# Optimization experiments

Hardware: AMD Instinct MI355X
Metric: run time of the kernel (lower is better)

## Reference

```python
import jax, jax.numpy as jnp
import numpy as np
from jax import lax

LEAK = 0.2
GN_EPS = 1e-5
K_NEIGH = 16
GROUPS = 4


def knn_idx(coor_k, coor_q, k):
    # coor_k: [B,Nk,3], coor_q: [B,Nq,3] -> [B,Nq,k] indices of k nearest in coor_k
    d = (jnp.sum(coor_q * coor_q, -1, keepdims=True)
         - 2.0 * jnp.einsum('bqc,bkc->bqk', coor_q, coor_k)
         + jnp.sum(coor_k * coor_k, -1)[:, None, :])
    _, idx = lax.top_k(-d, k)
    return idx


def graph_feature(coor_q, x_q, coor_k, x_k, k):
    # coor_*: [B,3,N*]; x_q: [B,C,Nq]; x_k: [B,C,Nk] -> [B,2C,Nq,k]
    idx = knn_idx(lax.stop_gradient(coor_k).transpose(0, 2, 1),
                  lax.stop_gradient(coor_q).transpose(0, 2, 1), k)
    B = x_k.shape[0]
    x_k_t = x_k.transpose(0, 2, 1)                      # [B,Nk,C]
    b_idx = jnp.arange(B)[:, None, None]
    nb = x_k_t[b_idx, idx]                              # [B,Nq,k,C]
    nb = nb.transpose(0, 3, 1, 2)                       # [B,C,Nq,k]
    xq = x_q[:, :, :, None]                             # [B,C,Nq,1]
    return jnp.concatenate([nb - xq, jnp.broadcast_to(xq, nb.shape)], axis=1)


def conv_gn_lrelu_max(f, w, gamma, beta):
    # f: [B,Cin,N,k]; w: [Cout,Cin] -> [B,Cout,N] (max over k)
    y = jnp.einsum('oc,bcnk->bonk', w, f)
    B, C, N, Kk = y.shape
    g = y.reshape(B, GROUPS, C // GROUPS, N, Kk)
    mu = g.mean((2, 3, 4), keepdims=True)
    var = g.var((2, 3, 4), keepdims=True)
    g = (g - mu) * lax.rsqrt(var + GN_EPS)
    y = g.reshape(B, C, N, Kk) * gamma[None, :, None, None] + beta[None, :, None, None]
    y = jnp.where(y >= 0, y, LEAK * y)
    return y.max(axis=-1)


def fps(xyz, n):
    # xyz: [B,N,3] -> [B,n] int32 (furthest point sampling, start at index 0)
    B, N, _ = xyz.shape
    d0 = jnp.sum((xyz - xyz[:, :1]) ** 2, -1)           # dist to point 0
    def body(dist, _):
        idx = jnp.argmax(dist, -1)                       # [B]
        nxt = jnp.take_along_axis(xyz, idx[:, None, None], 1)
        dist = jnp.minimum(dist, jnp.sum((xyz - nxt) ** 2, -1))
        return dist, idx
    _, idxs = lax.scan(body, d0, None, length=n - 1)     # [n-1,B]
    first = jnp.zeros((1, B), idxs.dtype)
    return jnp.concatenate([first, idxs], 0).T           # [B,n]


def fps_downsample(coor, x, n):
    # coor: [B,3,N], x: [B,C,N] -> ([B,3,n], [B,C,n])
    idx = fps(lax.stop_gradient(coor).transpose(0, 2, 1), n)
    comb = jnp.concatenate([coor, x], axis=1)            # [B,3+C,N]
    b_idx = jnp.arange(coor.shape[0])[:, None]
    new = comb.transpose(0, 2, 1)[b_idx, idx].transpose(0, 2, 1)
    return new[:, :3], new[:, 3:]


def setup_inputs() -> dict:
    key = jax.random.key(0)
    ks = jax.random.split(key, 16)
    s = 0.1
    return {
        'x': jax.random.normal(ks[0], (32, 2048, 3), jnp.float32),
        'w_in': jax.random.normal(ks[1], (8, 3), jnp.float32) * s,
        'b_in': jnp.zeros((8,), jnp.float32),
        'w1': jax.random.normal(ks[2], (32, 16), jnp.float32) * s,
        'g1': jnp.ones((32,), jnp.float32), 'be1': jnp.zeros((32,), jnp.float32),
        'w2': jax.random.normal(ks[3], (64, 64), jnp.float32) * s,
        'g2': jnp.ones((64,), jnp.float32), 'be2': jnp.zeros((64,), jnp.float32),
        'w3': jax.random.normal(ks[4], (64, 128), jnp.float32) * s,
        'g3': jnp.ones((64,), jnp.float32), 'be3': jnp.zeros((64,), jnp.float32),
        'w4': jax.random.normal(ks[5], (256, 128), jnp.float32) * s,
        'g4': jnp.ones((256,), jnp.float32), 'be4': jnp.zeros((256,), jnp.float32),
        'num0': 512,
        'num1': 128,
    }


def reference(x, w_in, b_in, w1, g1, be1, w2, g2, be2, w3, g3, be3, w4, g4, be4, num0, num1):
    coor = x.transpose(0, 2, 1)                          # [B,3,N]
    f = jnp.einsum('oc,bcn->bon', w_in, coor) + b_in[None, :, None]  # input_trans
    f = graph_feature(coor, f, coor, f, K_NEIGH)         # [B,16,N,k]
    f = conv_gn_lrelu_max(f, w1, g1, be1)                # [B,32,N]
    coor_q, f_q = fps_downsample(coor, f, num0)
    f = graph_feature(coor_q, f_q, coor, f, K_NEIGH)     # [B,64,num0,k]
    f = conv_gn_lrelu_max(f, w2, g2, be2)                # [B,64,num0]
    coor = coor_q
    f = graph_feature(coor, f, coor, f, K_NEIGH)         # [B,128,num0,k]
    f = conv_gn_lrelu_max(f, w3, g3, be3)                # [B,64,num0]
    coor_q, f_q = fps_downsample(coor, f, num1)
    f = graph_feature(coor_q, f_q, coor, f, K_NEIGH)     # [B,128,num1,k]
    f = conv_gn_lrelu_max(f, w4, g4, be4)                # [B,256,num1]
    coor = coor_q
    return coor.transpose(0, 2, 1), f.transpose(0, 2, 1)  # [B,num1,3], [B,num1,256]
```

## Files before the change

### kernel.cpp

```cpp
#include <hip/hip_runtime.h>

#define BB 32
#define NPTS0 2048
#define KNB 16
#define KC 256

constexpr int ilog2c(int n){ int l=0; while(n>1){ n>>=1; ++l; } return l; }

static __device__ __forceinline__ float sq3(float a, float b, float c){
  return __fadd_rn(__fadd_rn(__fmul_rn(a,a),__fmul_rn(b,b)),__fmul_rn(c,c));
}

template<int CTRL, int RM>
static __device__ __forceinline__ float dpp_maxf(float v){
  int s = __builtin_amdgcn_update_dpp(__float_as_int(v), __float_as_int(v), CTRL, RM, 0xF, false);
  return fmaxf(v, __int_as_float(s));
}
template<int CTRL, int RM>
static __device__ __forceinline__ unsigned dpp_minu(unsigned v){
  unsigned s = (unsigned)__builtin_amdgcn_update_dpp((int)v, (int)v, CTRL, RM, 0xF, false);
  return s < v ? s : v;
}

static __device__ __forceinline__ void proj_body(const float* __restrict__ x,
    const float* __restrict__ w, const float* __restrict__ bias, float* __restrict__ f0,
    int blk)
{
  int gid = blk*256 + threadIdx.x;
  if (gid >= BB*NPTS0) return;
  float x0 = x[gid*3+0], x1 = x[gid*3+1], x2 = x[gid*3+2];
  #pragma unroll
  for (int o = 0; o < 8; ++o){
    float acc = __fmul_rn(w[o*3+0], x0);
    acc = __fmaf_rn(w[o*3+1], x1, acc);
    acc = __fmaf_rn(w[o*3+2], x2, acc);
    f0[gid*8+o] = __fadd_rn(acc, bias[o]);
  }
}

#define KDECL(I) float th##I = __builtin_inff(); int ti##I = 0;
#define KINS(I,J) if (th##I < th##J){ float tv=th##I; th##I=th##J; th##J=tv; \
                                      int tj=ti##I; ti##I=ti##J; ti##J=tj; }
#define KST(I) pd[base+I] = th##I; pi[base+I] = (unsigned char)ti##I;

static __device__ __forceinline__ void knn_part_body(const float* __restrict__ qpts,
    const float* __restrict__ kpts, int Nq, int Nk, int nkc,
    float* __restrict__ pd, unsigned char* __restrict__ pi,
    int b, int qcb, int kc, float4* kk4)
{
  int tid = threadIdx.x;
  {
    int j = kc*KC + tid;
    float a = kpts[(b*Nk+j)*3+0];
    float c = kpts[(b*Nk+j)*3+1];
    float d = kpts[(b*Nk+j)*3+2];
    kk4[tid] = make_float4(a, c, d, sq3(a,c,d));
  }
  __syncthreads();
  int q = qcb*256 + tid;
  if (q >= Nq) return;
  float qx = qpts[(b*Nq+q)*3+0], qy = qpts[(b*Nq+q)*3+1], qz = qpts[(b*Nq+q)*3+2];
  float qq = sq3(qx,qy,qz);
  KDECL(0) KDECL(1) KDECL(2) KDECL(3) KDECL(4) KDECL(5) KDECL(6) KDECL(7)
  KDECL(8) KDECL(9) KDECL(10) KDECL(11) KDECL(12) KDECL(13) KDECL(14) KDECL(15)
  for (int j=0;j<KC;j++){
    float4 k4 = kk4[j];
    float dot = __fmul_rn(qx,k4.x);
    dot = __fmaf_rn(qy,k4.y,dot);
    dot = __fmaf_rn(qz,k4.z,dot);
    float d = __fadd_rn(__fsub_rn(qq, __fmul_rn(2.0f,dot)), k4.w);
    if (d < th15){
      th15 = d; ti15 = j;
      KINS(15,14) KINS(14,13) KINS(13,12) KINS(12,11) KINS(11,10) KINS(10,9)
      KINS(9,8) KINS(8,7) KINS(7,6) KINS(6,5) KINS(5,4) KINS(4,3) KINS(3,2)
      KINS(2,1) KINS(1,0)
    }
  }
  size_t base = ((size_t)(b*Nq+q)*nkc + kc)*KNB;
  KST(0) KST(1) KST(2) KST(3) KST(4) KST(5) KST(6) KST(7)
  KST(8) KST(9) KST(10) KST(11) KST(12) KST(13) KST(14) KST(15)
}

#define FPS_LOAD(T) float px##T, py##T, pz##T, d##T; { int i_=T*256+tid; \
  px##T=P[i_*3+0]; py##T=P[i_*3+1]; pz##T=P[i_*3+2]; \
  float dx_=__fsub_rn(px##T,c0x), dy_=__fsub_rn(py##T,c0y), dz_=__fsub_rn(pz##T,c0z); \
  d##T=sq3(dx_,dy_,dz_); bm=fmaxf(bm,d##T); }
#define FPS_MATCH(T) if (d##T == m_w) ci = (unsigned)(T*256 + tid);
#define FPS_OWN(T) if ((idx_w>>8) == T##u){ cx=px##T; cy=py##T; cz=pz##T; }
#define FPS_UPD(T) { float dx_=__fsub_rn(px##T,sx), dy_=__fsub_rn(py##T,sy), dz_=__fsub_rn(pz##T,sz); \
  float nd_=sq3(dx_,dy_,dz_); d##T=fminf(d##T,nd_); nbm=fmaxf(nbm,d##T); }

#define FPS_REDUCE_AND_PICK \
    float v = bm; \
    v = dpp_maxf<0x111, 0xF>(v); \
    v = dpp_maxf<0x112, 0xF>(v); \
    v = dpp_maxf<0x114, 0xF>(v); \
    v = dpp_maxf<0x118, 0xF>(v); \
    v = dpp_maxf<0x142, 0xA>(v); \
    v = dpp_maxf<0x143, 0xC>(v); \
    float m_w = __int_as_float(__builtin_amdgcn_readlane(__float_as_int(v), 63)); \
    unsigned ci = 0xFFFFFFFFu;

#define FPS_MIN_AND_MERGE \
    ci = dpp_minu<0x111, 0xF>(ci); \
    ci = dpp_minu<0x112, 0xF>(ci); \
    ci = dpp_minu<0x114, 0xF>(ci); \
    ci = dpp_minu<0x118, 0xF>(ci); \
    ci = dpp_minu<0x142, 0xA>(ci); \
    ci = dpp_minu<0x143, 0xC>(ci); \
    unsigned idx_w = (unsigned)__builtin_amdgcn_readlane((int)ci, 63); \
    int par = s & 1;

#define FPS_CROSSWAVE \
    __syncthreads(); \
    float4 q0 = *(const float4*)&swp[par][0][0]; float z0 = swp[par][0][4]; \
    float4 q1 = *(const float4*)&swp[par][1][0]; float z1 = swp[par][1][4]; \
    float4 q2 = *(const float4*)&swp[par][2][0]; float z2 = swp[par][2][4]; \
    float4 q3 = *(const float4*)&swp[par][3][0]; float z3 = swp[par][3][4]; \
    float mm = q0.x; unsigned mi = __float_as_uint(q0.y); \
    float sx = q0.z, sy = q0.w, sz = z0; \
    if (q1.x > mm || (q1.x == mm && __float_as_uint(q1.y) < mi)){ \
      mm = q1.x; mi = __float_as_uint(q1.y); sx = q1.z; sy = q1.w; sz = z1; } \
    if (q2.x > mm || (q2.x == mm && __float_as_uint(q2.y) < mi)){ \
      mm = q2.x; mi = __float_as_uint(q2.y); sx = q2.z; sy = q2.w; sz = z2; } \
    if (q3.x > mm || (q3.x == mm && __float_as_uint(q3.y) < mi)){ \
      mm = q3.x; mi = __float_as_uint(q3.y); sx = q3.z; sy = q3.w; sz = z3; } \
    if (tid == 0) oidx[b*S+s] = (int)mi;

static __device__ __forceinline__ void fps8_body(const float* __restrict__ pts,
    int S, int* __restrict__ oidx, int b, float* swpraw)
{
  float (*swp)[4][8] = reinterpret_cast<float(*)[4][8]>(swpraw);
  int tid = threadIdx.x, wid = tid >> 6;
  const float* P = pts + (size_t)b*2048*3;
  float c0x = P[0], c0y = P[1], c0z = P[2];
  float bm = -1.0f;
  FPS_LOAD(0) FPS_LOAD(1) FPS_LOAD(2) FPS_LOAD(3)
  FPS_LOAD(4) FPS_LOAD(5) FPS_LOAD(6) FPS_LOAD(7)
  if (tid == 0) oidx[b*S+0] = 0;
  for (int s=1; s<S; ++s){
    FPS_REDUCE_AND_PICK
    FPS_MATCH(7) FPS_MATCH(6) FPS_MATCH(5) FPS_MATCH(4)
    FPS_MATCH(3) FPS_MATCH(2) FPS_MATCH(1) FPS_MATCH(0)
    FPS_MIN_AND_MERGE
    if (tid == (int)(idx_w & 255u)){
      float cx = px0, cy = py0, cz = pz0;
      FPS_OWN(1) FPS_OWN(2) FPS_OWN(3) FPS_OWN(4) FPS_OWN(5) FPS_OWN(6) FPS_OWN(7)
      float4* wp = (float4*)&swp[par][wid][0];
      *wp = make_float4(m_w, __uint_as_float(idx_w), cx, cy);
      swp[par][wid][4] = cz;
    }
    FPS_CROSSWAVE
    float nbm = -1.0f;
    FPS_UPD(0) FPS_UPD(1) FPS_UPD(2) FPS_UPD(3)
    FPS_UPD(4) FPS_UPD(5) FPS_UPD(6) FPS_UPD(7)
    bm = nbm;
  }
}

static __device__ __forceinline__ void fps2_body(const float* __restrict__ pts,
    int S, int* __restrict__ oidx, int b, float* swpraw)
{
  float (*swp)[4][8] = reinterpret_cast<float(*)[4][8]>(swpraw);
  int tid = threadIdx.x, wid = tid >> 6;
  const float* P = pts + (size_t)b*512*3;
  float c0x = P[0], c0y = P[1], c0z = P[2];
  float bm = -1.0f;
  FPS_LOAD(0) FPS_LOAD(1)
  if (tid == 0) oidx[b*S+0] = 0;
  for (int s=1; s<S; ++s){
    FPS_REDUCE_AND_PICK
    FPS_MATCH(1) FPS_MATCH(0)
    FPS_MIN_AND_MERGE
    if (tid == (int)(idx_w & 255u)){
      float cx = px0, cy = py0, cz = pz0;
      FPS_OWN(1)
      float4* wp = (float4*)&swp[par][wid][0];
      *wp = make_float4(m_w, __uint_as_float(idx_w), cx, cy);
      swp[par][wid][4] = cz;
    }
    FPS_CROSSWAVE
    float nbm = -1.0f;
    FPS_UPD(0) FPS_UPD(1)
    bm = nbm;
  }
}

__global__ __launch_bounds__(256) void fused1_kernel(const float* __restrict__ x,
    const float* __restrict__ w_in, const float* __restrict__ b_in,
    float* __restrict__ f0, float* __restrict__ pd1, unsigned char* __restrict__ pi1,
    int* __restrict__ fidx0)
{
  __shared__ __align__(16) char sm[4096];
  int bid = blockIdx.x;
  if (bid < 32){
    fps8_body(x, 512, fidx0, bid, (float*)sm);
  } else if (bid < 32+2048){
    int r = bid - 32;
    int b = r & 31; int rest = r >> 5;
    knn_part_body(x, x, 2048, 2048, 8, pd1, pi1, b, rest & 7, rest >> 3, (float4*)sm);
  } else {
    proj_body(x, w_in, b_in, f0, bid - 2080);
  }
}

__global__ __launch_bounds__(256) void fused2_kernel(const float* __restrict__ coorq1,
    const float* __restrict__ x,
    float* __restrict__ pd2, unsigned char* __restrict__ pi2,
    float* __restrict__ pd3, unsigned char* __restrict__ pi3,
    int* __restrict__ fidx1)
{
  __shared__ __align__(16) char sm[4096];
  int bid = blockIdx.x;
  if (bid < 32){
    fps2_body(coorq1, 128, fidx1, bid, (float*)sm);
  } else if (bid < 32+512){
    int r = bid - 32;
    int b = r & 31; int rest = r >> 5;
    knn_part_body(coorq1, x, 512, 2048, 8, pd2, pi2, b, rest & 1, rest >> 1, (float4*)sm);
  } else {
    int r = bid - 544;
    int b = r & 31; int rest = r >> 5;
    knn_part_body(coorq1, coorq1, 512, 512, 2, pd3, pi3, b, rest & 1, rest >> 1, (float4*)sm);
  }
}

__global__ __launch_bounds__(256) void knn_part_kernel(const float* __restrict__ qpts,
    const float* __restrict__ kpts, int Nq, int Nk,
    float* __restrict__ pd, unsigned char* __restrict__ pi)
{
  __shared__ __align__(16) float4 kk4[KC];
  knn_part_body(qpts, kpts, Nq, Nk, gridDim.z, pd, pi,
                blockIdx.x, blockIdx.y, blockIdx.z, kk4);
}

__global__ __launch_bounds__(256) void knn_merge_kernel(const float* __restrict__ pd,
    const unsigned char* __restrict__ pi, int Nq, int nkc, int* __restrict__ oidx)
{
  int gid = blockIdx.x*256 + threadIdx.x;
  if (gid >= BB*Nq) return;
  float th[KNB]; int ti[KNB];
  #pragma unroll
  for (int i=0;i<KNB;i++){ th[i] = __builtin_inff(); ti[i] = 0; }
  size_t base = (size_t)gid*nkc*KNB;
  for (int kc=0;kc<nkc;kc++){
    size_t cb = base + (size_t)kc*KNB;
    for (int i=0;i<KNB;i++){
      float d = pd[cb+i];
      if (d >= th[KNB-1]) break;
      int j = kc*KC + (int)pi[cb+i];
      th[KNB-1] = d; ti[KNB-1] = j;
      #pragma unroll
      for (int m=KNB-1;m>0;--m){
        if (th[m] < th[m-1]){
          float tv=th[m]; th[m]=th[m-1]; th[m-1]=tv;
          int tj=ti[m]; ti[m]=ti[m-1]; ti[m-1]=tj;
        }
      }
    }
  }
  #pragma unroll
  for (int i=0;i<KNB;i++) oidx[gid*KNB + i] = ti[i];
}

template<int C, int O, bool DIFF>
__global__ __launch_bounds__(256) void gemv_kernel(const float* __restrict__ fin,
    const float* __restrict__ W, float* __restrict__ out, int Npts)
{
  constexpr int NT = O/8;
  constexpr int LNT = ilog2c(NT);
  int gid = blockIdx.x*256 + threadIdx.x;
  if (gid >= BB*Npts*NT) return;
  int tile = gid & (NT-1);
  int pn = gid >> LNT;
  const float* frow = fin + pn*C;
  float f[C];
  #pragma unroll
  for (int c=0;c<C;c++) f[c] = frow[c];
  float acc[8];
  const float* wbase = W + (tile*8)*(2*C);
  #pragma unroll
  for (int oo=0;oo<8;oo++){
    const float* wrow = wbase + oo*(2*C);
    float a = 0.f;
    #pragma unroll
    for (int c=0;c<C;c++){
      float wv = DIFF ? __fsub_rn(wrow[C+c], wrow[c]) : wrow[c];
      a = __fmaf_rn(wv, f[c], a);
    }
    acc[oo] = a;
  }
  float* orow = out + pn*O + tile*8;
  #pragma unroll
  for (int oo=0;oo<8;oo++) orow[oo] = acc[oo];
}

template<int O>
__global__ __launch_bounds__(256) void stats_kernel(const float* __restrict__ A,
    const float* __restrict__ Bq, const int* __restrict__ idx, int Nq, int Nk,
    double* __restrict__ part)
{
  constexpr int O4 = O/4;
  constexpr int LO4 = ilog2c(O4);
  int b = blockIdx.x, g = blockIdx.y, split = blockIdx.z;
  int nsplit = gridDim.z;
  int qlen = Nq / nsplit;
  int q0 = split * qlen;
  int tid = threadIdx.x;
  int total = qlen * KNB * O4;
  double s1 = 0.0, s2 = 0.0;
  for (int s = tid; s < total; s += 256){
    int oin = s & (O4-1);
    int rest = s >> LO4;
    int kk = rest & (KNB-1);
    int q = q0 + (rest >> 4);
    int j = idx[(b*Nq+q)*KNB + kk];
    float y = A[(b*Nk+j)*O + g*O4 + oin] + Bq[(b*Nq+q)*O + g*O4 + oin];
    s1 += (double)y;
    s2 += (double)y * (double)y;
  }
  #pragma unroll
  for (int m=32;m>0;m>>=1){ s1 += __shfl_down(s1,m); s2 += __shfl_down(s2,m); }
  __shared__ double sh1[4], sh2[4];
  int lane = tid & 63, w = tid >> 6;
  if (lane == 0){ sh1[w]=s1; sh2[w]=s2; }
  __syncthreads();
  if (tid == 0){
    double t1 = (sh1[0]+sh1[1])+(sh1[2]+sh1[3]);
    double t2 = (sh2[0]+sh2[1])+(sh2[2]+sh2[3]);
    int pi = (b*4+g)*nsplit + split;
    part[pi*2] = t1; part[pi*2+1] = t2;
  }
}

__global__ __launch_bounds__(128) void statsred_kernel(const double* __restrict__ part,
    int nsplit, double cnt, float* __restrict__ stats)
{
  int t = threadIdx.x;
  if (t >= BB*4) return;
  double s1=0.0, s2=0.0;
  for (int i=0;i<nsplit;i++){ s1 += part[(t*nsplit+i)*2]; s2 += part[(t*nsplit+i)*2+1]; }
  double mean = s1/cnt;
  double var = s2/cnt - mean*mean;
  double rstd = 1.0 / sqrt(var + 1e-5);
  stats[t*2] = (float)mean;
  stats[t*2+1] = (float)rstd;
}

template<int O>
__global__ __launch_bounds__(256) void final_kernel(const float* __restrict__ A,
    const float* __restrict__ Bq, const int* __restrict__ idx,
    const float* __restrict__ stats, const float* __restrict__ gamma,
    const float* __restrict__ beta, float* __restrict__ fout, int Nq, int Nk)
{
  constexpr int LO = ilog2c(O);
  constexpr int LO4 = ilog2c(O/4);
  int b = blockIdx.y;
  int t = blockIdx.x*256 + threadIdx.x;
  if (t >= Nq*O) return;
  int o = t & (O-1);
  int q = t >> LO;
  int g = o >> LO4;
  float mu   = stats[(b*4+g)*2];
  float rstd = stats[(b*4+g)*2+1];
  float gam = gamma[o], bet = beta[o];
  float bq = Bq[(b*Nq+q)*O + o];
  const int* ip = idx + (b*Nq+q)*KNB;
  float m = -__builtin_inff();
  #pragma unroll
  for (int kk=0;kk<KNB;kk++){
    int j = ip[kk];
    float y = A[(b*Nk+j)*O + o] + bq;
    float yn = __fmul_rn(__fsub_rn(y, mu), rstd);
    float yv = __fadd_rn(__fmul_rn(yn, gam), bet);
    float l = yv >= 0.f ? yv : 0.2f*yv;
    m = fmaxf(m, l);
  }
  fout[(b*Nq+q)*O + o] = m;
}

template<int C>
__global__ __launch_bounds__(256) void gather_kernel(const int* __restrict__ fidx,
    const float* __restrict__ pts, const float* __restrict__ fin,
    float* __restrict__ cq, float* __restrict__ fq, int Nin, int Nout)
{
  int gid = blockIdx.x*256 + threadIdx.x;
  if (gid >= BB*Nout) return;
  int b = gid / Nout;
  int i = gid - b*Nout;
  int src = fidx[b*Nout + i];
  #pragma unroll
  for (int c=0;c<3;c++) cq[gid*3+c] = pts[(b*Nin+src)*3+c];
  #pragma unroll
  for (int c=0;c<C;c++) fq[gid*C+c] = fin[(b*Nin+src)*C+c];
}

__global__ __launch_bounds__(256) void gatherc_kernel(const int* __restrict__ fidx,
    const float* __restrict__ pts, float* __restrict__ cq, int Nin, int Nout)
{
  int gid = blockIdx.x*256 + threadIdx.x;
  if (gid >= BB*Nout) return;
  int b = gid / Nout;
  int i = gid - b*Nout;
  int src = fidx[b*Nout + i];
  #pragma unroll
  for (int c=0;c<3;c++) cq[gid*3+c] = pts[(b*Nin+src)*3+c];
}

template<int C>
__global__ __launch_bounds__(256) void gatherf_kernel(const int* __restrict__ fidx,
    const float* __restrict__ fin, float* __restrict__ fq, int Nin, int Nout)
{
  int gid = blockIdx.x*256 + threadIdx.x;
  if (gid >= BB*Nout) return;
  int b = gid / Nout;
  int i = gid - b*Nout;
  int src = fidx[b*Nout + i];
  #pragma unroll
  for (int c=0;c<C;c++) fq[gid*C+c] = fin[(b*Nin+src)*C+c];
}

extern "C" void kernel_launch(void* const* d_in, const int* in_sizes, int n_in,
                              void* d_out, int out_size, void* d_ws, size_t ws_size,
                              hipStream_t stream)
{
  (void)in_sizes; (void)n_in; (void)out_size; (void)ws_size;
  const float* x    = (const float*)d_in[0];
  const float* w_in = (const float*)d_in[1];
  const float* b_in = (const float*)d_in[2];
  const float* w1 = (const float*)d_in[3];
  const float* g1 = (const float*)d_in[4];
  const float* be1= (const float*)d_in[5];
  const float* w2 = (const float*)d_in[6];
  const float* g2 = (const float*)d_in[7];
  const float* be2= (const float*)d_in[8];
  const float* w3 = (const float*)d_in[9];
  const float* g3 = (const float*)d_in[10];
  const float* be3= (const float*)d_in[11];
  const float* w4 = (const float*)d_in[12];
  const float* g4 = (const float*)d_in[13];
  const float* be4= (const float*)d_in[14];

  float* out = (float*)d_out;
  float* coor_out = out;
  float* f_out = out + BB*128*3;

  char* ws = (char*)d_ws;
  size_t off = 0;
  auto alloc = [&](size_t bytes)->void*{ void* p = ws + off; off += (bytes + 255) & ~(size_t)255; return p; };

  float* f0     = (float*)alloc((size_t)BB*2048*8*4);
  int*   idx1   = (int*)  alloc((size_t)BB*2048*16*4);
  float* f1     = (float*)alloc((size_t)BB*2048*32*4);
  double* part  = (double*)alloc((size_t)BB*4*8*2*8);
  float* statsv = (float*)alloc((size_t)BB*4*2*4);
  int*   fidx0  = (int*)  alloc((size_t)BB*512*4);
  float* coorq1 = (float*)alloc((size_t)BB*512*3*4);
  float* fq1    = (float*)alloc((size_t)BB*512*32*4);
  int*   idx2   = (int*)  alloc((size_t)BB*512*16*4);
  float* f2     = (float*)alloc((size_t)BB*512*64*4);
  int*   idx3   = (int*)  alloc((size_t)BB*512*16*4);
  float* f3     = (float*)alloc((size_t)BB*512*64*4);
  int*   fidx1  = (int*)  alloc((size_t)BB*128*4);
  float* fq2    = (float*)alloc((size_t)BB*128*64*4);
  int*   idx4   = (int*)  alloc((size_t)BB*128*16*4);
  float* pd2          = (float*)alloc((size_t)BB*512*8*KNB*4);
  unsigned char* pi2  = (unsigned char*)alloc((size_t)BB*512*8*KNB);
  float* pd3          = (float*)alloc((size_t)BB*512*2*KNB*4);
  unsigned char* pi3  = (unsigned char*)alloc((size_t)BB*512*2*KNB);
  float* pd4          = (float*)alloc((size_t)BB*128*2*KNB*4);
  unsigned char* pi4  = (unsigned char*)alloc((size_t)BB*128*2*KNB);

  char* U = (char*)alloc((size_t)48<<20);
  float* pd1         = (float*)U;
  unsigned char* pi1 = (unsigned char*)(U + ((size_t)34<<20));
  float* A  = (float*)U;
  float* Bq = (float*)(U + ((size_t)20<<20));

  auto cdiv = [](int a, int b){ return (a+b-1)/b; };

  fused1_kernel<<<2336,256,0,stream>>>(x, w_in, b_in, f0, pd1, pi1, fidx0);

  knn_merge_kernel<<<cdiv(BB*2048,256),256,0,stream>>>(pd1, pi1, 2048, 8, idx1);
  gemv_kernel<8,32,false><<<cdiv(BB*2048*4,256),256,0,stream>>>(f0, w1, A, 2048);
  gemv_kernel<8,32,true ><<<cdiv(BB*2048*4,256),256,0,stream>>>(f0, w1, Bq, 2048);
  stats_kernel<32><<<dim3(BB,4,8),256,0,stream>>>(A, Bq, idx1, 2048, 2048, part);
  statsred_kernel<<<1,128,0,stream>>>(part, 8, 8.0*2048*16, statsv);
  final_kernel<32><<<dim3(cdiv(2048*32,256),BB),256,0,stream>>>(A, Bq, idx1, statsv, g1, be1, f1, 2048, 2048);

  gather_kernel<32><<<cdiv(BB*512,256),256,0,stream>>>(fidx0, x, f1, coorq1, fq1, 2048, 512);

  fused2_kernel<<<672,256,0,stream>>>(coorq1, x, pd2, pi2, pd3, pi3, fidx1);

  knn_merge_kernel<<<cdiv(BB*512,256),256,0,stream>>>(pd2, pi2, 512, 8, idx2);
  knn_merge_kernel<<<cdiv(BB*512,256),256,0,stream>>>(pd3, pi3, 512, 2, idx3);

  gatherc_kernel<<<cdiv(BB*128,256),256,0,stream>>>(fidx1, coorq1, coor_out, 512, 128);
  knn_part_kernel<<<dim3(BB,1,2),256,0,stream>>>(coor_out, coorq1, 128, 512, pd4, pi4);
  knn_merge_kernel<<<cdiv(BB*128,256),256,0,stream>>>(pd4, pi4, 128, 2, idx4);

  gemv_kernel<32,64,false><<<cdiv(BB*2048*8,256),256,0,stream>>>(f1, w2, A, 2048);
  gemv_kernel<32,64,true ><<<cdiv(BB*512*8,256),256,0,stream>>>(fq1, w2, Bq, 512);
  stats_kernel<64><<<dim3(BB,4,8),256,0,stream>>>(A, Bq, idx2, 512, 2048, part);
  statsred_kernel<<<1,128,0,stream>>>(part, 8, 16.0*512*16, statsv);
  final_kernel<64><<<dim3(cdiv(512*64,256),BB),256,0,stream>>>(A, Bq, idx2, statsv, g2, be2, f2, 512, 2048);

  gemv_kernel<64,64,false><<<cdiv(BB*512*8,256),256,0,stream>>>(f2, w3, A, 512);
  gemv_kernel<64,64,true ><<<cdiv(BB*512*8,256),256,0,stream>>>(f2, w3, Bq, 512);
  stats_kernel<64><<<dim3(BB,4,8),256,0,stream>>>(A, Bq, idx3, 512, 512, part);
  statsred_kernel<<<1,128,0,stream>>>(part, 8, 16.0*512*16, statsv);
  final_kernel<64><<<dim3(cdiv(512*64,256),BB),256,0,stream>>>(A, Bq, idx3, statsv, g3, be3, f3, 512, 512);

  gatherf_kernel<64><<<cdiv(BB*128,256),256,0,stream>>>(fidx1, f3, fq2, 512, 128);
  gemv_kernel<64,256,false><<<cdiv(BB*512*32,256),256,0,stream>>>(f3, w4, A, 512);
  gemv_kernel<64,256,true ><<<cdiv(BB*128*32,256),256,0,stream>>>(fq2, w4, Bq, 128);
  stats_kernel<256><<<dim3(BB,4,8),256,0,stream>>>(A, Bq, idx4, 128, 512, part);
  statsred_kernel<<<1,128,0,stream>>>(part, 8, 64.0*128*16, statsv);
  final_kernel<256><<<dim3(cdiv(128*256,256),BB),256,0,stream>>>(A, Bq, idx4, statsv, g4, be4, f_out, 128, 512);
}
```

Baseline: 1.438 ms.

## Run furthest point sampling in a single wavefront with LDS coordinate lookup

Rewrites the FPS bodies so one 64-lane wave holds all points in registers (32 or 8 per lane) and stores coordinates in LDS, removing the per-step block barrier and cross-wave merge. The selected point's coordinates are fetched from LDS by index instead of being broadcast by the owning thread. This lengthens the per-step serial work per lane and enlarges shared memory in the fused kernels, and launch bounds now request one block per SM, which may limit occupancy for the co-scheduled kNN blocks.

```diff
diff --git a/kernel.cpp b/kernel.cpp
--- a/kernel.cpp
+++ b/kernel.cpp
@@ -81,147 +81,122 @@
   KST(8) KST(9) KST(10) KST(11) KST(12) KST(13) KST(14) KST(15)
 }
 
-#define FPS_LOAD(T) float px##T, py##T, pz##T, d##T; { int i_=T*256+tid; \
-  px##T=P[i_*3+0]; py##T=P[i_*3+1]; pz##T=P[i_*3+2]; \
+#define REP8(M)  M(0) M(1) M(2) M(3) M(4) M(5) M(6) M(7)
+#define REP8D(M) M(7) M(6) M(5) M(4) M(3) M(2) M(1) M(0)
+#define REP32(M) REP8(M) M(8) M(9) M(10) M(11) M(12) M(13) M(14) M(15) \
+  M(16) M(17) M(18) M(19) M(20) M(21) M(22) M(23) \
+  M(24) M(25) M(26) M(27) M(28) M(29) M(30) M(31)
+#define REP32D(M) M(31) M(30) M(29) M(28) M(27) M(26) M(25) M(24) \
+  M(23) M(22) M(21) M(20) M(19) M(18) M(17) M(16) \
+  M(15) M(14) M(13) M(12) M(11) M(10) M(9) M(8) REP8D(M)
+
+#define F1_LOAD(T) float px##T, py##T, pz##T, d##T; { int i_ = T*64 + lane; \
+  px##T = P[i_*3+0]; py##T = P[i_*3+1]; pz##T = P[i_*3+2]; \
+  lds4[i_] = make_float4(px##T, py##T, pz##T, 0.f); \
   float dx_=__fsub_rn(px##T,c0x), dy_=__fsub_rn(py##T,c0y), dz_=__fsub_rn(pz##T,c0z); \
-  d##T=sq3(dx_,dy_,dz_); bm=fmaxf(bm,d##T); }
-#define FPS_MATCH(T) if (d##T == m_w) ci = (unsigned)(T*256 + tid);
-#define FPS_OWN(T) if ((idx_w>>8) == T##u){ cx=px##T; cy=py##T; cz=pz##T; }
-#define FPS_UPD(T) { float dx_=__fsub_rn(px##T,sx), dy_=__fsub_rn(py##T,sy), dz_=__fsub_rn(pz##T,sz); \
-  float nd_=sq3(dx_,dy_,dz_); d##T=fminf(d##T,nd_); nbm=fmaxf(nbm,d##T); }
-
-#define FPS_REDUCE_AND_PICK \
+  d##T = sq3(dx_,dy_,dz_); bm = fmaxf(bm, d##T); }
+#define F1_MATCH(T) if (d##T == m_w) ci = (unsigned)(T*64 + lane);
+#define F1_UPD(T) { float dx_=__fsub_rn(px##T,sx), dy_=__fsub_rn(py##T,sy), dz_=__fsub_rn(pz##T,sz); \
+  float nd_=sq3(dx_,dy_,dz_); d##T=fminf(d##T,nd_); bm=fmaxf(bm,d##T); }
+
+#define F1_REDUCE_MAX \
     float v = bm; \
-    v = dpp_maxf<0x111, 0xF>(v); \
-    v = dpp_maxf<0x112, 0xF>(v); \
-    v = dpp_maxf<0x114, 0xF>(v); \
-    v = dpp_maxf<0x118, 0xF>(v); \
-    v = dpp_maxf<0x142, 0xA>(v); \
-    v = dpp_maxf<0x143, 0xC>(v); \
+    v = dpp_maxf<0x111,0xF>(v); \
+    v = dpp_maxf<0x112,0xF>(v); \
+    v = dpp_maxf<0x114,0xF>(v); \
+    v = dpp_maxf<0x118,0xF>(v); \
+    v = dpp_maxf<0x142,0xA>(v); \
+    v = dpp_maxf<0x143,0xC>(v); \
     float m_w = __int_as_float(__builtin_amdgcn_readlane(__float_as_int(v), 63)); \
     unsigned ci = 0xFFFFFFFFu;
 
-#define FPS_MIN_AND_MERGE \
-    ci = dpp_minu<0x111, 0xF>(ci); \
-    ci = dpp_minu<0x112, 0xF>(ci); \
-    ci = dpp_minu<0x114, 0xF>(ci); \
-    ci = dpp_minu<0x118, 0xF>(ci); \
-    ci = dpp_minu<0x142, 0xA>(ci); \
-    ci = dpp_minu<0x143, 0xC>(ci); \
-    unsigned idx_w = (unsigned)__builtin_amdgcn_readlane((int)ci, 63); \
-    int par = s & 1;
-
-#define FPS_CROSSWAVE \
-    __syncthreads(); \
-    float4 q0 = *(const float4*)&swp[par][0][0]; float z0 = swp[par][0][4]; \
-    float4 q1 = *(const float4*)&swp[par][1][0]; float z1 = swp[par][1][4]; \
-    float4 q2 = *(const float4*)&swp[par][2][0]; float z2 = swp[par][2][4]; \
-    float4 q3 = *(const float4*)&swp[par][3][0]; float z3 = swp[par][3][4]; \
-    float mm = q0.x; unsigned mi = __float_as_uint(q0.y); \
-    float sx = q0.z, sy = q0.w, sz = z0; \
-    if (q1.x > mm || (q1.x == mm && __float_as_uint(q1.y) < mi)){ \
-      mm = q1.x; mi = __float_as_uint(q1.y); sx = q1.z; sy = q1.w; sz = z1; } \
-    if (q2.x > mm || (q2.x == mm && __float_as_uint(q2.y) < mi)){ \
-      mm = q2.x; mi = __float_as_uint(q2.y); sx = q2.z; sy = q2.w; sz = z2; } \
-    if (q3.x > mm || (q3.x == mm && __float_as_uint(q3.y) < mi)){ \
-      mm = q3.x; mi = __float_as_uint(q3.y); sx = q3.z; sy = q3.w; sz = z3; } \
-    if (tid == 0) oidx[b*S+s] = (int)mi;
-
-static __device__ __forceinline__ void fps8_body(const float* __restrict__ pts,
-    int S, int* __restrict__ oidx, int b, float* swpraw)
-{
-  float (*swp)[4][8] = reinterpret_cast<float(*)[4][8]>(swpraw);
-  int tid = threadIdx.x, wid = tid >> 6;
+#define F1_REDUCE_MIN \
+    ci = dpp_minu<0x111,0xF>(ci); \
+    ci = dpp_minu<0x112,0xF>(ci); \
+    ci = dpp_minu<0x114,0xF>(ci); \
+    ci = dpp_minu<0x118,0xF>(ci); \
+    ci = dpp_minu<0x142,0xA>(ci); \
+    ci = dpp_minu<0x143,0xC>(ci); \
+    unsigned idx_w = (unsigned)__builtin_amdgcn_readlane((int)ci, 63);
+
+static __device__ __forceinline__ void fps_w32_body(const float* __restrict__ pts,
+    int S, int* __restrict__ oidx, int b, float4* lds4)
+{
+  int lane = threadIdx.x & 63;
   const float* P = pts + (size_t)b*2048*3;
   float c0x = P[0], c0y = P[1], c0z = P[2];
   float bm = -1.0f;
-  FPS_LOAD(0) FPS_LOAD(1) FPS_LOAD(2) FPS_LOAD(3)
-  FPS_LOAD(4) FPS_LOAD(5) FPS_LOAD(6) FPS_LOAD(7)
-  if (tid == 0) oidx[b*S+0] = 0;
+  REP32(F1_LOAD)
+  if (lane == 0) oidx[b*S+0] = 0;
   for (int s=1; s<S; ++s){
-    FPS_REDUCE_AND_PICK
-    FPS_MATCH(7) FPS_MATCH(6) FPS_MATCH(5) FPS_MATCH(4)
-    FPS_MATCH(3) FPS_MATCH(2) FPS_MATCH(1) FPS_MATCH(0)
-    FPS_MIN_AND_MERGE
-    if (tid == (int)(idx_w & 255u)){
-      float cx = px0, cy = py0, cz = pz0;
-      FPS_OWN(1) FPS_OWN(2) FPS_OWN(3) FPS_OWN(4) FPS_OWN(5) FPS_OWN(6) FPS_OWN(7)
-      float4* wp = (float4*)&swp[par][wid][0];
-      *wp = make_float4(m_w, __uint_as_float(idx_w), cx, cy);
-      swp[par][wid][4] = cz;
-    }
-    FPS_CROSSWAVE
-    float nbm = -1.0f;
-    FPS_UPD(0) FPS_UPD(1) FPS_UPD(2) FPS_UPD(3)
-    FPS_UPD(4) FPS_UPD(5) FPS_UPD(6) FPS_UPD(7)
-    bm = nbm;
-  }
-}
-
-static __device__ __forceinline__ void fps2_body(const float* __restrict__ pts,
-    int S, int* __restrict__ oidx, int b, float* swpraw)
-{
-  float (*swp)[4][8] = reinterpret_cast<float(*)[4][8]>(swpraw);
-  int tid = threadIdx.x, wid = tid >> 6;
+    F1_REDUCE_MAX
+    REP32D(F1_MATCH)
+    F1_REDUCE_MIN
+    if (lane == 0) oidx[b*S+s] = (int)idx_w;
+    float4 c = lds4[idx_w];
+    float sx = c.x, sy = c.y, sz = c.z;
+    bm = -1.0f;
+    REP32(F1_UPD)
+  }
+}
+
+static __device__ __forceinline__ void fps_w8_body(const float* __restrict__ pts,
+    int S, int* __restrict__ oidx, int b, float4* lds4)
+{
+  int lane = threadIdx.x & 63;
   const float* P = pts + (size_t)b*512*3;
   float c0x = P[0], c0y = P[1], c0z = P[2];
   float bm = -1.0f;
-  FPS_LOAD(0) FPS_LOAD(1)
-  if (tid == 0) oidx[b*S+0] = 0;
+  REP8(F1_LOAD)
+  if (lane == 0) oidx[b*S+0] = 0;
   for (int s=1; s<S; ++s){
-    FPS_REDUCE_AND_PICK
-    FPS_MATCH(1) FPS_MATCH(0)
-    FPS_MIN_AND_MERGE
-    if (tid == (int)(idx_w & 255u)){
-      float cx = px0, cy = py0, cz = pz0;
-      FPS_OWN(1)
-      float4* wp = (float4*)&swp[par][wid][0];
-      *wp = make_float4(m_w, __uint_as_float(idx_w), cx, cy);
-      swp[par][wid][4] = cz;
-    }
-    FPS_CROSSWAVE
-    float nbm = -1.0f;
-    FPS_UPD(0) FPS_UPD(1)
-    bm = nbm;
-  }
-}
-
-__global__ __launch_bounds__(256) void fused1_kernel(const float* __restrict__ x,
+    F1_REDUCE_MAX
+    REP8D(F1_MATCH)
+    F1_REDUCE_MIN
+    if (lane == 0) oidx[b*S+s] = (int)idx_w;
+    float4 c = lds4[idx_w];
+    float sx = c.x, sy = c.y, sz = c.z;
+    bm = -1.0f;
+    REP8(F1_UPD)
+  }
+}
+
+__global__ __launch_bounds__(256, 1) void fused1_kernel(const float* __restrict__ x,
     const float* __restrict__ w_in, const float* __restrict__ b_in,
     float* __restrict__ f0, float* __restrict__ pd1, unsigned char* __restrict__ pi1,
     int* __restrict__ fidx0)
 {
-  __shared__ __align__(16) char sm[4096];
+  __shared__ __align__(16) float4 sm4[2048];
   int bid = blockIdx.x;
   if (bid < 32){
-    fps8_body(x, 512, fidx0, bid, (float*)sm);
+    if (threadIdx.x < 64) fps_w32_body(x, 512, fidx0, bid, sm4);
   } else if (bid < 32+2048){
     int r = bid - 32;
     int b = r & 31; int rest = r >> 5;
-    knn_part_body(x, x, 2048, 2048, 8, pd1, pi1, b, rest & 7, rest >> 3, (float4*)sm);
+    knn_part_body(x, x, 2048, 2048, 8, pd1, pi1, b, rest & 7, rest >> 3, sm4);
   } else {
     proj_body(x, w_in, b_in, f0, bid - 2080);
   }
 }
 
-__global__ __launch_bounds__(256) void fused2_kernel(const float* __restrict__ coorq1,
+__global__ __launch_bounds__(256, 1) void fused2_kernel(const float* __restrict__ coorq1,
     const float* __restrict__ x,
     float* __restrict__ pd2, unsigned char* __restrict__ pi2,
     float* __restrict__ pd3, unsigned char* __restrict__ pi3,
     int* __restrict__ fidx1)
 {
-  __shared__ __align__(16) char sm[4096];
+  __shared__ __align__(16) float4 sm4[512];
   int bid = blockIdx.x;
   if (bid < 32){
-    fps2_body(coorq1, 128, fidx1, bid, (float*)sm);
+    if (threadIdx.x < 64) fps_w8_body(coorq1, 128, fidx1, bid, sm4);
   } else if (bid < 32+512){
     int r = bid - 32;
     int b = r & 31; int rest = r >> 5;
-    knn_part_body(coorq1, x, 512, 2048, 8, pd2, pi2, b, rest & 1, rest >> 1, (float4*)sm);
+    knn_part_body(coorq1, x, 512, 2048, 8, pd2, pi2, b, rest & 1, rest >> 1, sm4);
   } else {
     int r = bid - 544;
     int b = r & 31; int rest = r >> 5;
-    knn_part_body(coorq1, coorq1, 512, 512, 2, pd3, pi3, b, rest & 1, rest >> 1, (float4*)sm);
+    knn_part_body(coorq1, coorq1, 512, 512, 2, pd3, pi3, b, rest & 1, rest >> 1, sm4);
   }
 }
 
```

Measured after the change: 1.601 ms. +11.4%, slower.
